# Kernel tuning notes

Measured on AMD Instinct MI355X. Metric: run time of the kernel, lower is better.

Reference implementation:

```python
import jax, jax.numpy as jnp
import numpy as np

N = 4096        # total nodes per batched graph
E_EDGES = 65536 # edges per graph (avg degree 16)
B = 16          # graphs in batch
NFEAT = 1280
NHID = 512
NHEAD = 8
DFF = 2048      # TransformerEncoderLayer default dim_feedforward
HD = NHID // NHEAD
LN_EPS = 1e-5


def setup_inputs() -> dict:
    key = jax.random.key(0)
    ks = jax.random.split(key, 32)
    s = 0.02
    inp = {}
    inp["fea1"] = jax.random.normal(ks[0], (N, NFEAT), jnp.float32)
    inp["fea2"] = jax.random.normal(ks[1], (N, NFEAT), jnp.float32)
    inp["src1"] = jax.random.randint(ks[2], (E_EDGES,), 0, N, jnp.int32)
    inp["dst1"] = jax.random.randint(ks[3], (E_EDGES,), 0, N, jnp.int32)
    inp["src2"] = jax.random.randint(ks[4], (E_EDGES,), 0, N, jnp.int32)
    inp["dst2"] = jax.random.randint(ks[5], (E_EDGES,), 0, N, jnp.int32)
    seg = ((jnp.arange(N) * B) // N).astype(jnp.int32)  # equal-size graphs, sorted ids
    inp["seg1"] = seg
    inp["seg2"] = seg
    inp["num_graphs"] = B
    # GraphConv params (torch Linear convention: y = x @ W.T + b)
    inp["W1"] = jax.random.normal(ks[6], (NHID, NFEAT), jnp.float32) * s
    inp["b1"] = jnp.zeros((NHID,), jnp.float32)
    inp["W2"] = jax.random.normal(ks[7], (NHID, NHID), jnp.float32) * s
    inp["b2"] = jnp.zeros((NHID,), jnp.float32)
    # TransformerEncoderLayer params
    inp["in_proj_w"] = jax.random.normal(ks[8], (3 * NHID, NHID), jnp.float32) * s
    inp["in_proj_b"] = jnp.zeros((3 * NHID,), jnp.float32)
    inp["out_proj_w"] = jax.random.normal(ks[9], (NHID, NHID), jnp.float32) * s
    inp["out_proj_b"] = jnp.zeros((NHID,), jnp.float32)
    inp["ln1_g"] = jnp.ones((NHID,), jnp.float32)
    inp["ln1_b"] = jnp.zeros((NHID,), jnp.float32)
    inp["ln2_g"] = jnp.ones((NHID,), jnp.float32)
    inp["ln2_b"] = jnp.zeros((NHID,), jnp.float32)
    inp["ff1_w"] = jax.random.normal(ks[10], (DFF, NHID), jnp.float32) * s
    inp["ff1_b"] = jnp.zeros((DFF,), jnp.float32)
    inp["ff2_w"] = jax.random.normal(ks[11], (NHID, DFF), jnp.float32) * s
    inp["ff2_b"] = jnp.zeros((NHID,), jnp.float32)
    # MLP head
    inp["l1_w"] = jax.random.normal(ks[12], (512, NHID), jnp.float32) * s
    inp["l1_b"] = jnp.zeros((512,), jnp.float32)
    inp["l2_w"] = jax.random.normal(ks[13], (128, 512), jnp.float32) * s
    inp["l2_b"] = jnp.zeros((128,), jnp.float32)
    inp["l3_w"] = jax.random.normal(ks[14], (2, 128), jnp.float32) * s
    inp["l3_b"] = jnp.zeros((2,), jnp.float32)
    return inp


def graph_conv(fea, src, dst, W, b):
    # DGL GraphConv, norm='both': D_in^{-1/2} A D_out^{-1/2} X W + b (W applied pre-agg)
    ones = jnp.ones(src.shape[0], fea.dtype)
    deg_out = jnp.maximum(jax.ops.segment_sum(ones, src, num_segments=N), 1.0)
    deg_in = jnp.maximum(jax.ops.segment_sum(ones, dst, num_segments=N), 1.0)
    h = fea * (deg_out ** -0.5)[:, None]
    h = h @ W.T  # [N, nhid]
    agg = jax.ops.segment_sum(h[src], dst, num_segments=N)  # scatter-add over edges
    return agg * (deg_in ** -0.5)[:, None] + b


def layer_norm(x, g, b):
    mu = jnp.mean(x, -1, keepdims=True)
    var = jnp.mean((x - mu) ** 2, -1, keepdims=True)
    return (x - mu) * jax.lax.rsqrt(var + LN_EPS) * g + b


def encoder_layer(x, in_proj_w, in_proj_b, out_proj_w, out_proj_b,
                  ln1_g, ln1_b, ln2_g, ln2_b, ff1_w, ff1_b, ff2_w, ff2_b):
    # post-norm TransformerEncoderLayer, unbatched [S, E] input, eval mode (no dropout)
    qkv = x @ in_proj_w.T + in_proj_b               # [S, 3E]
    q, k, v = jnp.split(qkv, 3, axis=-1)
    S = x.shape[0]
    q = q.reshape(S, NHEAD, HD).transpose(1, 0, 2)  # [H, S, hd]
    k = k.reshape(S, NHEAD, HD).transpose(1, 0, 2)
    v = v.reshape(S, NHEAD, HD).transpose(1, 0, 2)
    scores = jnp.einsum('hqd,hkd->hqk', q, k) / jnp.sqrt(jnp.float32(HD))
    attn = jax.nn.softmax(scores, axis=-1)
    ctx = jnp.einsum('hqk,hkd->hqd', attn, v).transpose(1, 0, 2).reshape(S, NHID)
    x = layer_norm(x + (ctx @ out_proj_w.T + out_proj_b), ln1_g, ln1_b)
    ff = jax.nn.relu(x @ ff1_w.T + ff1_b) @ ff2_w.T + ff2_b
    return layer_norm(x + ff, ln2_g, ln2_b)


def mean_nodes(fea, seg, num_graphs):
    counts = jnp.maximum(jax.ops.segment_sum(jnp.ones(fea.shape[0], fea.dtype), seg, num_segments=num_graphs), 1.0)
    return jax.ops.segment_sum(fea, seg, num_segments=num_graphs) / counts[:, None]


def reference(fea1, fea2, W1, b1, W2, b2, in_proj_w, in_proj_b, out_proj_w, out_proj_b,
              ln1_g, ln1_b, ln2_g, ln2_b, ff1_w, ff1_b, ff2_w, ff2_b,
              l1_w, l1_b, l2_w, l2_b, l3_w, l3_b,
              src1, dst1, src2, dst2, seg1, seg2, num_graphs):
    tparams = (in_proj_w, in_proj_b, out_proj_w, out_proj_b,
               ln1_g, ln1_b, ln2_g, ln2_b, ff1_w, ff1_b, ff2_w, ff2_b)
    h1 = jax.nn.relu(graph_conv(fea1, src1, dst1, W1, b1))
    h2 = jax.nn.relu(graph_conv(fea2, src2, dst2, W1, b1))
    h1 = encoder_layer(h1, *tparams)
    h2 = encoder_layer(h2, *tparams)
    h1 = jax.nn.relu(graph_conv(h1, src1, dst1, W2, b2))
    h2 = jax.nn.relu(graph_conv(h2, src2, dst2, W2, b2))
    hg = mean_nodes(h1, seg1, num_graphs) * mean_nodes(h2, seg2, num_graphs)  # [B, nhid]
    out = hg @ l1_w.T + l1_b          # note: original has NO activation between l1/l2/l3
    out = out @ l2_w.T + l2_b
    return jax.nn.softmax(out @ l3_w.T + l3_b, axis=-1)
```

## Files before the change

kernel.cpp:

```cpp
#include <hip/hip_runtime.h>
#include <math.h>

#define NN 4096
#define EE 65536
#define NS 8192
#define NFEAT 1280
#define NHID 512
#define DFF 2048

typedef unsigned short u16;
typedef unsigned int u32;
typedef __attribute__((ext_vector_type(8))) short bf16x8;
typedef __attribute__((ext_vector_type(4))) float f32x4;
#define MFMA16(A,B,C) __builtin_amdgcn_mfma_f32_16x16x32_bf16(A,B,C,0,0,0)
#define GAS __attribute__((address_space(1)))
#define LAS __attribute__((address_space(3)))

static const size_t OFF_A   = 0ull;
static const size_t OFF_HP  = 8388608ull;
static const size_t OFF_X   = 12582912ull;
static const size_t OFF_XB  = 16777216ull;
static const size_t OFF_E   = 18874368ull;
static const size_t OFF_VT  = 25165824ull;
static const size_t OFF_CTB = 27262976ull;
static const size_t OFF_W1B = 29360128ull;
static const size_t OFF_IPB = 29687808ull;
static const size_t OFF_OPB = 30081024ull;
static const size_t OFF_F1B = 30212096ull;
static const size_t OFF_F2B = 30736384ull;
static const size_t OFF_W2B = 31260672ull;
static const size_t OFF_ME  = 31391744ull;
static const size_t OFF_DG  = 31408128ull;
static const size_t OFF_INT = 31424512ull;

#define IH_S1 0
#define IH_D1 4096
#define IH_S2 8192
#define IH_D2 12288
#define IO_F1 16384
#define IO_F2 20608
#define IC_1  24832
#define IC_2  28928
#define IE_1  33024
#define IE_2  98560

__device__ __forceinline__ u16 f2b(float x) {
    u32 u = __float_as_uint(x);
    return (u16)((u + 0x7fffu + ((u >> 16) & 1u)) >> 16);
}
__device__ __forceinline__ float b_lo(u32 u) { return __uint_as_float(u << 16); }
__device__ __forceinline__ float b_hi(u32 u) { return __uint_as_float(u & 0xffff0000u); }

__global__ __launch_bounds__(256) void k_hist(const int* __restrict__ s1, const int* __restrict__ d1,
                                              const int* __restrict__ s2, const int* __restrict__ d2,
                                              int* __restrict__ I)
{
    int e = blockIdx.x * 256 + threadIdx.x;
    if (e < EE) {
        atomicAdd(&I[IH_S1 + s1[e]], 1);
        atomicAdd(&I[IH_D1 + d1[e]], 1);
        atomicAdd(&I[IH_S2 + s2[e]], 1);
        atomicAdd(&I[IH_D2 + d2[e]], 1);
    }
}

__global__ __launch_bounds__(256) void k_deg_fin(const int* __restrict__ I, float* __restrict__ deg)
{
    int i = blockIdx.x * 256 + threadIdx.x;
    if (i < 4 * NN) deg[i] = rsqrtf(fmaxf((float)I[i], 1.0f));
}

__global__ __launch_bounds__(256) void k_scan(int* __restrict__ I)
{
    int b = blockIdx.x;
    const int* hist = I + (b ? IH_D2 : IH_D1);
    int* offs = I + (b ? IO_F2 : IO_F1);
    int* cur  = I + (b ? IC_2 : IC_1);
    __shared__ int part[256];
    int t = threadIdx.x;
    int base = t * 16;
    int loc[16];
    int s = 0;
#pragma unroll
    for (int i = 0; i < 16; ++i) { loc[i] = s; s += hist[base + i]; }
    part[t] = s;
    __syncthreads();
    if (t == 0) {
        int a = 0;
        for (int i = 0; i < 256; ++i) { int v = part[i]; part[i] = a; a += v; }
        offs[NN] = a;
    }
    __syncthreads();
    int p = part[t];
#pragma unroll
    for (int i = 0; i < 16; ++i) { offs[base + i] = p + loc[i]; cur[base + i] = p + loc[i]; }
}

__global__ __launch_bounds__(256) void k_fill(const int* __restrict__ s1, const int* __restrict__ d1,
                                              const int* __restrict__ s2, const int* __restrict__ d2,
                                              int* __restrict__ I)
{
    int e = blockIdx.x * 256 + threadIdx.x;
    if (e < EE) {
        int p1 = atomicAdd(&I[IC_1 + d1[e]], 1);
        I[IE_1 + p1] = s1[e];
        int p2 = atomicAdd(&I[IC_2 + d2[e]], 1);
        I[IE_2 + p2] = s2[e];
    }
}

__global__ __launch_bounds__(256) void k_cvt(const float* __restrict__ src, u16* __restrict__ dst, int n)
{
    int i = (blockIdx.x * 256 + threadIdx.x) * 8;
    if (i >= n) return;
    float4 a = *(const float4*)&src[i];
    float4 b = *(const float4*)&src[i + 4];
    uint4 o;
    o.x = (u32)f2b(a.x) | ((u32)f2b(a.y) << 16);
    o.y = (u32)f2b(a.z) | ((u32)f2b(a.w) << 16);
    o.z = (u32)f2b(b.x) | ((u32)f2b(b.y) << 16);
    o.w = (u32)f2b(b.z) | ((u32)f2b(b.w) << 16);
    *(uint4*)&dst[i] = o;
}

__global__ __launch_bounds__(256) void k_scale_bf(const float* __restrict__ in1, const float* __restrict__ in2,
                                                  const float* __restrict__ sc1, const float* __restrict__ sc2,
                                                  u16* __restrict__ out, int ncol)
{
    int quads = ncol >> 2;
    long long idx = (long long)blockIdx.x * 256 + threadIdx.x;
    if (idx >= (long long)NS * quads) return;
    int r  = (int)(idx / quads);
    int cq = (int)(idx % quads) * 4;
    const float* in; const float* sc; int rr;
    if (r < NN) { in = in1; sc = sc1; rr = r; } else { in = in2; sc = sc2; rr = r - NN; }
    float4 v = *(const float4*)&in[(size_t)rr * ncol + cq];
    float s = sc[rr];
    uint2 o;
    o.x = (u32)f2b(v.x * s) | ((u32)f2b(v.y * s) << 16);
    o.y = (u32)f2b(v.z * s) | ((u32)f2b(v.w * s) << 16);
    *(uint2*)&out[(size_t)r * ncol + cq] = o;
}

__global__ __launch_bounds__(256) void k_gemm_bf(const u16* __restrict__ A, const u16* __restrict__ W,
                                                 const float* __restrict__ bias, float* __restrict__ Cf,
                                                 u16* __restrict__ Cb, int M, int N, int K, int relu)
{
    __shared__ u16 As[128 * 32];
    __shared__ u16 Bs[128 * 32];
    int t = threadIdx.x;
    int w = t >> 6, L = t & 63;
    int lm = L & 15, lq = L >> 4;
    int wr = w >> 1, wc = w & 1;
    int row0 = blockIdx.y * 128, col0 = blockIdx.x * 128;
    f32x4 acc[4][4];
#pragma unroll
    for (int i = 0; i < 4; ++i)
#pragma unroll
        for (int j = 0; j < 4; ++j) acc[i][j] = (f32x4){0.f, 0.f, 0.f, 0.f};

    int sr = t >> 2;
    int sk = (t & 3) * 8;
    const u16* Ag = &A[(size_t)row0 * K + sk];
    const u16* Wg = &W[(size_t)col0 * K + sk];

    for (int k0 = 0; k0 < K; k0 += 32) {
        uint4 a0 = *(const uint4*)&Ag[(size_t)sr * K + k0];
        uint4 a1 = *(const uint4*)&Ag[(size_t)(sr + 64) * K + k0];
        uint4 b0 = *(const uint4*)&Wg[(size_t)sr * K + k0];
        uint4 b1 = *(const uint4*)&Wg[(size_t)(sr + 64) * K + k0];
        __syncthreads();
        *(uint4*)&As[sr * 32 + sk] = a0;
        *(uint4*)&As[(sr + 64) * 32 + sk] = a1;
        *(uint4*)&Bs[sr * 32 + sk] = b0;
        *(uint4*)&Bs[(sr + 64) * 32 + sk] = b1;
        __syncthreads();
        bf16x8 af[4], bw[4];
#pragma unroll
        for (int i = 0; i < 4; ++i) {
            af[i] = *(const bf16x8*)&As[(wr * 64 + i * 16 + lm) * 32 + lq * 8];
            bw[i] = *(const bf16x8*)&Bs[(wc * 64 + i * 16 + lm) * 32 + lq * 8];
        }
#pragma unroll
        for (int i = 0; i < 4; ++i)
#pragma unroll
            for (int j = 0; j < 4; ++j)
                acc[i][j] = MFMA16(af[i], bw[j], acc[i][j]);
    }

#pragma unroll
    for (int i = 0; i < 4; ++i) {
        int row = row0 + wr * 64 + i * 16 + lq * 4;
#pragma unroll
        for (int j = 0; j < 4; ++j) {
            int col = col0 + wc * 64 + j * 16 + lm;
            float bv = bias ? bias[col] : 0.0f;
#pragma unroll
            for (int r = 0; r < 4; ++r) {
                float v = acc[i][j][r] + bv;
                if (relu) v = fmaxf(v, 0.0f);
                size_t off = (size_t)(row + r) * N + col;
                if (Cb) Cb[off] = f2b(v);
                else    Cf[off] = v;
            }
        }
    }
}

__global__ __launch_bounds__(256) void k_gather_bf(const u16* __restrict__ hp, const int* __restrict__ I,
                                                   const float* __restrict__ din1, const float* __restrict__ din2,
                                                   const float* __restrict__ bias,
                                                   float* __restrict__ xout, u16* __restrict__ xb)
{
    int r = blockIdx.x, c = threadIdx.x;
    int g = r >> 12, rl = r & (NN - 1);
    const int* off = I + (g ? IO_F2 : IO_F1);
    const int* eid = I + (g ? IE_2 : IE_1);
    int beg = off[rl], end = off[rl + 1];
    const u16* base = hp + ((size_t)g << 12) * NHID;
    float a0 = 0.f, a1 = 0.f;
    for (int i = beg; i < end; ++i) {
        u32 v = ((const u32*)(base + (size_t)eid[i] * NHID))[c];
        a0 += b_lo(v);
        a1 += b_hi(v);
    }
    float s = (g ? din2 : din1)[rl];
    float2 bv = *(const float2*)&bias[c * 2];
    float v0 = fmaxf(fmaf(a0, s, bv.x), 0.f);
    float v1 = fmaxf(fmaf(a1, s, bv.y), 0.f);
    size_t o = (size_t)r * NHID + c * 2;
    if (xout) *(float2*)&xout[o] = make_float2(v0, v1);
    if (xb) *(u32*)&xb[o] = (u32)f2b(v0) | ((u32)f2b(v1) << 16);
}

__global__ __launch_bounds__(256) void k_vtrans(const u16* __restrict__ qkvb, u16* __restrict__ vtb)
{
    __shared__ u16 tile[64][65];
    int t = threadIdx.x;
    int kt = blockIdx.x, h = blockIdx.y, g = blockIdx.z;
    int k0 = kt * 64;
    size_t gbase = (size_t)g * NN;
#pragma unroll
    for (int p = 0; p < 4; ++p) {
        int kl = p * 16 + (t >> 4);
        int d  = (t & 15) * 4;
        uint2 v = *(const uint2*)&qkvb[(gbase + k0 + kl) * 1536 + 1024 + h * 64 + d];
        tile[kl][d + 0] = (u16)(v.x & 0xffff);
        tile[kl][d + 1] = (u16)(v.x >> 16);
        tile[kl][d + 2] = (u16)(v.y & 0xffff);
        tile[kl][d + 3] = (u16)(v.y >> 16);
    }
    __syncthreads();
#pragma unroll
    for (int p = 0; p < 4; ++p) {
        int dl = p * 16 + (t >> 4);
        int k4 = (t & 15) * 4;
        u16 v0 = tile[k4 + 0][dl];
        u16 v1 = tile[k4 + 1][dl];
        u16 v2 = tile[k4 + 2][dl];
        u16 v3 = tile[k4 + 3][dl];
        uint2 o;
        o.x = (u32)v0 | ((u32)v1 << 16);
        o.y = (u32)v2 | ((u32)v3 << 16);
        *(uint2*)&vtb[((size_t)(g * 8 + h) * 64 + dl) * (size_t)NN + k0 + k4] = o;
    }
}

__global__ __launch_bounds__(256, 2) void k_attn(const u16* __restrict__ qkv,
                                                 const u16* __restrict__ vt,
                                                 u16* __restrict__ ctb)
{
    __shared__ __align__(16) u16 Kl[2][32 * 64];
    __shared__ __align__(16) u16 Vl[2][64 * 32];
    __shared__ __align__(16) u16 Pl[4][32 * 40];
    int t = threadIdx.x;
    int w = t >> 6, L = t & 63;
    int lm = L & 15, lq = L >> 4;
    int qt = blockIdx.x, h = blockIdx.y, g = blockIdx.z;
    size_t gbase = (size_t)g * NN;
    int q0 = qt * 128 + w * 32;

    const u16* kbase = &qkv[gbase * 1536 + 512 + h * 64];
    const u16* vbase = &vt[(size_t)(g * 8 + h) * 64 * (size_t)NN];

    int krow = t >> 3;
    int kbyt = ((t & 7) * 16) ^ ((krow & 7) << 4);
    const u16* kg = &kbase[(size_t)krow * 1536 + (kbyt >> 1)];
    int vrow = t >> 2;
    int vbyt = ((t & 3) * 16) ^ ((vrow & 3) << 4);
    const u16* vg = &vbase[(size_t)vrow * NN + (vbyt >> 1)];
    u16* Pw = &Pl[w][0];

    bf16x8 qa[2][2];
#pragma unroll
    for (int qg = 0; qg < 2; ++qg) {
        const u16* qp = &qkv[(gbase + q0 + qg * 16 + lm) * 1536 + h * 64 + lq * 8];
        qa[qg][0] = *(const bf16x8*)qp;
        qa[qg][1] = *(const bf16x8*)(qp + 32);
    }
    f32x4 ctx[2][4];
#pragma unroll
    for (int qg = 0; qg < 2; ++qg)
#pragma unroll
        for (int n = 0; n < 4; ++n) ctx[qg][n] = (f32x4){0.f, 0.f, 0.f, 0.f};
    float m[2][4], lsum[2][4];
#pragma unroll
    for (int qg = 0; qg < 2; ++qg)
#pragma unroll
        for (int r = 0; r < 4; ++r) { m[qg][r] = -1e30f; lsum[qg][r] = 0.0f; }

    __builtin_amdgcn_global_load_lds((const GAS void*)kg, (LAS void*)((LAS char*)&Kl[0][0] + w * 1024), 16, 0, 0);
    __builtin_amdgcn_global_load_lds((const GAS void*)vg, (LAS void*)((LAS char*)&Vl[0][0] + w * 1024), 16, 0, 0);
    __syncthreads();

    int cur = 0;
    for (int t0 = 0; t0 < NN; t0 += 32) {
        if (t0 + 32 < NN) {
            __builtin_amdgcn_global_load_lds((const GAS void*)(kg + (size_t)(t0 + 32) * 1536),
                                             (LAS void*)((LAS char*)&Kl[cur ^ 1][0] + w * 1024), 16, 0, 0);
            __builtin_amdgcn_global_load_lds((const GAS void*)(vg + (t0 + 32)),
                                             (LAS void*)((LAS char*)&Vl[cur ^ 1][0] + w * 1024), 16, 0, 0);
        }
        const char* Kc = (const char*)&Kl[cur][0];
        const char* Vc = (const char*)&Vl[cur][0];
        bf16x8 kb[2][2], vb[4];
#pragma unroll
        for (int kc = 0; kc < 2; ++kc) {
            int row = kc * 16 + lm;
            int sw = (row & 7) << 4;
            const char* rp = Kc + row * 128;
            kb[kc][0] = *(const bf16x8*)(rp + ((lq * 16) ^ sw));
            kb[kc][1] = *(const bf16x8*)(rp + ((64 + lq * 16) ^ sw));
        }
#pragma unroll
        for (int n = 0; n < 4; ++n) {
            int row = n * 16 + lm;
            vb[n] = *(const bf16x8*)(Vc + row * 64 + ((lq * 16) ^ ((row & 3) << 4)));
        }

        f32x4 s[2][2];
        __builtin_amdgcn_s_setprio(1);
#pragma unroll
        for (int kc = 0; kc < 2; ++kc)
#pragma unroll
            for (int qg = 0; qg < 2; ++qg) {
                f32x4 z = (f32x4){0.f, 0.f, 0.f, 0.f};
                z = MFMA16(qa[qg][0], kb[kc][0], z);
                z = MFMA16(qa[qg][1], kb[kc][1], z);
                s[qg][kc] = z * 0.125f;
            }
        __builtin_amdgcn_s_setprio(0);

        float dmax = -1e30f;
#pragma unroll
        for (int qg = 0; qg < 2; ++qg)
#pragma unroll
            for (int r = 0; r < 4; ++r)
                dmax = fmaxf(dmax, fmaxf(s[qg][0][r], s[qg][1][r]) - m[qg][r]);
        if (__any(dmax > 8.0f)) {
#pragma unroll
            for (int qg = 0; qg < 2; ++qg)
#pragma unroll
                for (int r = 0; r < 4; ++r) {
                    float mr = fmaxf(s[qg][0][r], s[qg][1][r]);
                    mr = fmaxf(mr, __shfl_xor(mr, 1));
                    mr = fmaxf(mr, __shfl_xor(mr, 2));
                    mr = fmaxf(mr, __shfl_xor(mr, 4));
                    mr = fmaxf(mr, __shfl_xor(mr, 8));
                    float mn = fmaxf(m[qg][r], mr);
                    float corr = __expf(m[qg][r] - mn);
                    m[qg][r] = mn;
                    lsum[qg][r] *= corr;
#pragma unroll
                    for (int n = 0; n < 4; ++n) ctx[qg][n][r] *= corr;
                }
        }
#pragma unroll
        for (int qg = 0; qg < 2; ++qg)
#pragma unroll
            for (int r = 0; r < 4; ++r) {
                float p0 = __expf(s[qg][0][r] - m[qg][r]);
                float p1 = __expf(s[qg][1][r] - m[qg][r]);
                lsum[qg][r] += p0 + p1;
                int row = qg * 16 + lq * 4 + r;
                Pw[row * 40 + lm] = f2b(p0);
                Pw[row * 40 + 16 + lm] = f2b(p1);
            }

        __builtin_amdgcn_s_setprio(1);
#pragma unroll
        for (int qg = 0; qg < 2; ++qg) {
            bf16x8 pa = *(const bf16x8*)&Pw[(qg * 16 + lm) * 40 + lq * 8];
#pragma unroll
            for (int n = 0; n < 4; ++n)
                ctx[qg][n] = MFMA16(pa, vb[n], ctx[qg][n]);
        }
        __builtin_amdgcn_s_setprio(0);

        __syncthreads();
        cur ^= 1;
    }

#pragma unroll
    for (int qg = 0; qg < 2; ++qg) {
        float inv[4];
#pragma unroll
        for (int r = 0; r < 4; ++r) {
            float lr = lsum[qg][r];
            lr += __shfl_xor(lr, 1);
            lr += __shfl_xor(lr, 2);
            lr += __shfl_xor(lr, 4);
            lr += __shfl_xor(lr, 8);
            inv[r] = 1.0f / lr;
        }
#pragma unroll
        for (int n = 0; n < 4; ++n)
#pragma unroll
            for (int r = 0; r < 4; ++r) {
                int row = q0 + qg * 16 + lq * 4 + r;
                int col = h * 64 + n * 16 + lm;
                ctb[(gbase + row) * NHID + col] = f2b(ctx[qg][n][r] * inv[r]);
            }
    }
}

__global__ __launch_bounds__(256) void k_add_ln(const float* __restrict__ x, const float* __restrict__ y,
                                                const float* __restrict__ g, const float* __restrict__ bb,
                                                float* __restrict__ xout, u16* __restrict__ xb,
                                                const float* __restrict__ sc1, const float* __restrict__ sc2)
{
    int r = blockIdx.x, tid = threadIdx.x;
    int c = tid * 2;
    float2 xv = *(const float2*)&x[(size_t)r * NHID + c];
    float2 yv = *(const float2*)&y[(size_t)r * NHID + c];
    float a0 = xv.x + yv.x, a1 = xv.y + yv.y;
    float s = a0 + a1;
    float qs = a0 * a0 + a1 * a1;
#pragma unroll
    for (int off = 32; off > 0; off >>= 1) {
        s  += __shfl_xor(s, off);
        qs += __shfl_xor(qs, off);
    }
    __shared__ float ss[4], qq[4];
    int w = tid >> 6;
    if ((tid & 63) == 0) { ss[w] = s; qq[w] = qs; }
    __syncthreads();
    s  = ss[0] + ss[1] + ss[2] + ss[3];
    qs = qq[0] + qq[1] + qq[2] + qq[3];
    float mu  = s * (1.0f / NHID);
    float var = qs * (1.0f / NHID) - mu * mu;
    float rs = rsqrtf(var + 1e-5f);
    float2 gv = *(const float2*)&g[c];
    float2 bv = *(const float2*)&bb[c];
    float o0 = (a0 - mu) * rs * gv.x + bv.x;
    float o1 = (a1 - mu) * rs * gv.y + bv.y;
    if (xout) *(float2*)&xout[(size_t)r * NHID + c] = make_float2(o0, o1);
    float sc = 1.0f;
    if (sc1) sc = (r < NN) ? sc1[r] : sc2[r - NN];
    u32 o = (u32)f2b(o0 * sc) | ((u32)f2b(o1 * sc) << 16);
    *(u32*)&xb[(size_t)r * NHID + c] = o;
}

__global__ __launch_bounds__(512) void k_seg_mean(const float* __restrict__ h, float* __restrict__ means)
{
    int b = blockIdx.x;
    int st = blockIdx.y;
    int col = threadIdx.x;
    const float* hp = &h[((size_t)st * NN + (size_t)b * 256) * NHID + col];
    float acc = 0.0f;
    for (int i = 0; i < 256; ++i) acc += hp[(size_t)i * NHID];
    means[((size_t)st * 16 + b) * NHID + col] = acc * (1.0f / 256.0f);
}

__global__ __launch_bounds__(256) void k_head(const float* __restrict__ means,
                                              const float* __restrict__ l1w, const float* __restrict__ l1b,
                                              const float* __restrict__ l2w, const float* __restrict__ l2b,
                                              const float* __restrict__ l3w, const float* __restrict__ l3b,
                                              float* __restrict__ out)
{
    __shared__ float hg[512];
    __shared__ float t1[512];
    __shared__ float t2[128];
    int b = blockIdx.x;
    int t = threadIdx.x;
    hg[t]       = means[b * 512 + t]       * means[(16 + b) * 512 + t];
    hg[t + 256] = means[b * 512 + t + 256] * means[(16 + b) * 512 + t + 256];
    __syncthreads();
#pragma unroll
    for (int o = t; o < 512; o += 256) {
        const float* wr = &l1w[(size_t)o * 512];
        float acc = l1b[o];
        for (int k = 0; k < 512; k += 4) {
            float4 w = *(const float4*)&wr[k];
            acc = fmaf(hg[k], w.x, acc);
            acc = fmaf(hg[k + 1], w.y, acc);
            acc = fmaf(hg[k + 2], w.z, acc);
            acc = fmaf(hg[k + 3], w.w, acc);
        }
        t1[o] = acc;
    }
    __syncthreads();
    if (t < 128) {
        const float* wr = &l2w[(size_t)t * 512];
        float acc = l2b[t];
        for (int k = 0; k < 512; k += 4) {
            float4 w = *(const float4*)&wr[k];
            acc = fmaf(t1[k], w.x, acc);
            acc = fmaf(t1[k + 1], w.y, acc);
            acc = fmaf(t1[k + 2], w.z, acc);
            acc = fmaf(t1[k + 3], w.w, acc);
        }
        t2[t] = acc;
    }
    __syncthreads();
    if (t < 64) {
        float p0 = t2[t] * l3w[t] + t2[t + 64] * l3w[t + 64];
        float p1 = t2[t] * l3w[128 + t] + t2[t + 64] * l3w[128 + t + 64];
#pragma unroll
        for (int off = 32; off > 0; off >>= 1) {
            p0 += __shfl_xor(p0, off);
            p1 += __shfl_xor(p1, off);
        }
        if (t == 0) {
            float v0 = p0 + l3b[0], v1 = p1 + l3b[1];
            float mx = fmaxf(v0, v1);
            float e0 = __expf(v0 - mx), e1 = __expf(v1 - mx);
            float inv = 1.0f / (e0 + e1);
            out[b * 2 + 0] = e0 * inv;
            out[b * 2 + 1] = e1 * inv;
        }
    }
}

extern "C" void kernel_launch(void* const* d_in, const int* in_sizes, int n_in,
                              void* d_out, int out_size, void* d_ws, size_t ws_size,
                              hipStream_t stream)
{
    const float* fea1 = (const float*)d_in[0];
    const float* fea2 = (const float*)d_in[1];
    const int* src1 = (const int*)d_in[2];
    const int* dst1 = (const int*)d_in[3];
    const int* src2 = (const int*)d_in[4];
    const int* dst2 = (const int*)d_in[5];
    const float* W1 = (const float*)d_in[9];
    const float* b1 = (const float*)d_in[10];
    const float* W2 = (const float*)d_in[11];
    const float* b2 = (const float*)d_in[12];
    const float* in_proj_w = (const float*)d_in[13];
    const float* in_proj_b = (const float*)d_in[14];
    const float* out_proj_w = (const float*)d_in[15];
    const float* out_proj_b = (const float*)d_in[16];
    const float* ln1_g = (const float*)d_in[17];
    const float* ln1_b = (const float*)d_in[18];
    const float* ln2_g = (const float*)d_in[19];
    const float* ln2_b = (const float*)d_in[20];
    const float* ff1_w = (const float*)d_in[21];
    const float* ff1_b = (const float*)d_in[22];
    const float* ff2_w = (const float*)d_in[23];
    const float* ff2_b = (const float*)d_in[24];
    const float* l1_w = (const float*)d_in[25];
    const float* l1_b = (const float*)d_in[26];
    const float* l2_w = (const float*)d_in[27];
    const float* l2_b = (const float*)d_in[28];
    const float* l3_w = (const float*)d_in[29];
    const float* l3_b = (const float*)d_in[30];

    float* ws = (float*)d_ws;
    u16*  Ab   = (u16*)(ws + OFF_A);
    float* HP  = ws + OFF_HP;
    u16*  HPb  = (u16*)(ws + OFF_HP);
    float* X   = ws + OFF_X;
    u16*  Xb   = (u16*)(ws + OFF_XB);
    u16*  QKVb = (u16*)(ws + OFF_E);
    float* AG2 = ws + OFF_E;
    u16*  Vtb  = (u16*)(ws + OFF_VT);
    u16*  CTb  = (u16*)(ws + OFF_CTB);
    u16*  W1b  = (u16*)(ws + OFF_W1B);
    u16*  IPb  = (u16*)(ws + OFF_IPB);
    u16*  OPb  = (u16*)(ws + OFF_OPB);
    u16*  F1b  = (u16*)(ws + OFF_F1B);
    u16*  F2b  = (u16*)(ws + OFF_F2B);
    u16*  W2b  = (u16*)(ws + OFF_W2B);
    float* ME  = ws + OFF_ME;
    float* DG  = ws + OFF_DG;
    int*   I   = (int*)(ws + OFF_INT);
    float* dout1 = DG;
    float* din1  = DG + NN;
    float* dout2 = DG + 2 * NN;
    float* din2  = DG + 3 * NN;

    hipMemsetAsync(I, 0, 4 * NN * sizeof(int), stream);

    k_hist<<<EE / 256, 256, 0, stream>>>(src1, dst1, src2, dst2, I);
    k_deg_fin<<<(4 * NN) / 256, 256, 0, stream>>>(I, DG);
    k_scan<<<2, 256, 0, stream>>>(I);
    k_fill<<<EE / 256, 256, 0, stream>>>(src1, dst1, src2, dst2, I);

    k_cvt<<<(NHID * NFEAT / 8 + 255) / 256, 256, 0, stream>>>(W1, W1b, NHID * NFEAT);
    k_cvt<<<(3 * NHID * NHID / 8 + 255) / 256, 256, 0, stream>>>(in_proj_w, IPb, 3 * NHID * NHID);
    k_cvt<<<(NHID * NHID / 8 + 255) / 256, 256, 0, stream>>>(out_proj_w, OPb, NHID * NHID);
    k_cvt<<<(DFF * NHID / 8 + 255) / 256, 256, 0, stream>>>(ff1_w, F1b, DFF * NHID);
    k_cvt<<<(NHID * DFF / 8 + 255) / 256, 256, 0, stream>>>(ff2_w, F2b, NHID * DFF);
    k_cvt<<<(NHID * NHID / 8 + 255) / 256, 256, 0, stream>>>(W2, W2b, NHID * NHID);

    {
        long long tq = (long long)NS * (NFEAT / 4);
        k_scale_bf<<<(int)((tq + 255) / 256), 256, 0, stream>>>(fea1, fea2, dout1, dout2, Ab, NFEAT);
    }
    k_gemm_bf<<<dim3(NHID / 128, NS / 128), 256, 0, stream>>>(Ab, W1b, nullptr, nullptr, HPb, NS, NHID, NFEAT, 0);
    k_gather_bf<<<NS, 256, 0, stream>>>(HPb, I, din1, din2, b1, X, Xb);

    k_gemm_bf<<<dim3(1536 / 128, NS / 128), 256, 0, stream>>>(Xb, IPb, in_proj_b, nullptr, QKVb, NS, 1536, NHID, 0);
    k_vtrans<<<dim3(NN / 64, 8, 2), 256, 0, stream>>>(QKVb, Vtb);
    k_attn<<<dim3(NN / 128, 8, 2), 256, 0, stream>>>(QKVb, Vtb, CTb);
    k_gemm_bf<<<dim3(NHID / 128, NS / 128), 256, 0, stream>>>(CTb, OPb, out_proj_b, HP, nullptr, NS, NHID, NHID, 0);
    k_add_ln<<<NS, 256, 0, stream>>>(X, HP, ln1_g, ln1_b, X, Xb, nullptr, nullptr);
    k_gemm_bf<<<dim3(DFF / 128, NS / 128), 256, 0, stream>>>(Xb, F1b, ff1_b, nullptr, Ab, NS, DFF, NHID, 1);
    k_gemm_bf<<<dim3(NHID / 128, NS / 128), 256, 0, stream>>>(Ab, F2b, ff2_b, HP, nullptr, NS, NHID, DFF, 0);
    k_add_ln<<<NS, 256, 0, stream>>>(X, HP, ln2_g, ln2_b, nullptr, Ab, dout1, dout2);

    k_gemm_bf<<<dim3(NHID / 128, NS / 128), 256, 0, stream>>>(Ab, W2b, nullptr, nullptr, HPb, NS, NHID, NHID, 0);
    k_gather_bf<<<NS, 256, 0, stream>>>(HPb, I, din1, din2, b2, AG2, nullptr);

    k_seg_mean<<<dim3(16, 2), 512, 0, stream>>>(AG2, ME);
    k_head<<<16, 256, 0, stream>>>(ME, l1_w, l1_b, l2_w, l2_b, l3_w, l3_b, (float*)d_out);
}
```

Measured before the change: 674.7 us.

## Widen attention KV tile, use exp2 softmax, async LDS GEMM loads, 64-wide tiles

The attention kernel now processes 64 keys per iteration instead of 32. It folds log2(e) into the score scale so it can use exp2f, and writes P with packed bf16 stores into a swizzled 128-byte-row layout. The GEMM switches from register-staged LDS stores to global_load_lds direct copies and gains a BN=64 template variant, used for the N=512 outputs to put more blocks on the GPU. The V transpose reorders keys to match the new K/V staging layout. The aim is fewer barriers and loop overheads plus better occupancy, at the cost of more LDS per attention block and a GEMM that is still single-buffered.

```diff
diff --git a/kernel.cpp b/kernel.cpp
--- a/kernel.cpp
+++ b/kernel.cpp
@@ -1,4 +1,5 @@
 #include <hip/hip_runtime.h>
+#include <hip/hip_bf16.h>
 #include <math.h>
 
 #define NN 4096
@@ -15,6 +16,9 @@
 #define MFMA16(A,B,C) __builtin_amdgcn_mfma_f32_16x16x32_bf16(A,B,C,0,0,0)
 #define GAS __attribute__((address_space(1)))
 #define LAS __attribute__((address_space(3)))
+
+#define SCL 0.18033688011112042f
+#define THR 11.541560327111707f
 
 static const size_t OFF_A   = 0ull;
 static const size_t OFF_HP  = 8388608ull;
@@ -142,55 +146,58 @@
     *(uint2*)&out[(size_t)r * ncol + cq] = o;
 }
 
+template<int BN>
 __global__ __launch_bounds__(256) void k_gemm_bf(const u16* __restrict__ A, const u16* __restrict__ W,
                                                  const float* __restrict__ bias, float* __restrict__ Cf,
                                                  u16* __restrict__ Cb, int M, int N, int K, int relu)
 {
+    constexpr int RM = (BN == 128) ? 4 : 2;
     __shared__ u16 As[128 * 32];
-    __shared__ u16 Bs[128 * 32];
+    __shared__ u16 Bs[BN * 32];
     int t = threadIdx.x;
     int w = t >> 6, L = t & 63;
     int lm = L & 15, lq = L >> 4;
-    int wr = w >> 1, wc = w & 1;
-    int row0 = blockIdx.y * 128, col0 = blockIdx.x * 128;
-    f32x4 acc[4][4];
-#pragma unroll
-    for (int i = 0; i < 4; ++i)
+    int wr = (BN == 128) ? (w >> 1) : w;
+    int wc = (BN == 128) ? (w & 1) : 0;
+    int row0 = blockIdx.y * 128, col0 = blockIdx.x * BN;
+    f32x4 acc[RM][4];
+#pragma unroll
+    for (int i = 0; i < RM; ++i)
 #pragma unroll
         for (int j = 0; j < 4; ++j) acc[i][j] = (f32x4){0.f, 0.f, 0.f, 0.f};
 
-    int sr = t >> 2;
-    int sk = (t & 3) * 8;
-    const u16* Ag = &A[(size_t)row0 * K + sk];
-    const u16* Wg = &W[(size_t)col0 * K + sk];
+    const u16* As0 = &A[(size_t)(row0 + (w * 2) * 16 + (L >> 2)) * K + (L & 3) * 8];
+    const u16* As1 = As0 + (size_t)16 * K;
+    const u16* Bs0 = &W[(size_t)(col0 + ((BN == 128) ? (w * 2) * 16 : w * 16) + (L >> 2)) * K + (L & 3) * 8];
+    const u16* Bs1 = Bs0 + (size_t)16 * K;
+    u16* AsW = &As[(w * 2) * 512];
+    u16* BsW = (BN == 128) ? &Bs[(w * 2) * 512] : &Bs[w * 512];
 
     for (int k0 = 0; k0 < K; k0 += 32) {
-        uint4 a0 = *(const uint4*)&Ag[(size_t)sr * K + k0];
-        uint4 a1 = *(const uint4*)&Ag[(size_t)(sr + 64) * K + k0];
-        uint4 b0 = *(const uint4*)&Wg[(size_t)sr * K + k0];
-        uint4 b1 = *(const uint4*)&Wg[(size_t)(sr + 64) * K + k0];
+        if (k0) __syncthreads();
+        __builtin_amdgcn_global_load_lds((const GAS void*)(As0 + k0), (LAS void*)(LAS char*)AsW, 16, 0, 0);
+        __builtin_amdgcn_global_load_lds((const GAS void*)(As1 + k0), (LAS void*)((LAS char*)AsW + 1024), 16, 0, 0);
+        __builtin_amdgcn_global_load_lds((const GAS void*)(Bs0 + k0), (LAS void*)(LAS char*)BsW, 16, 0, 0);
+        if constexpr (BN == 128)
+            __builtin_amdgcn_global_load_lds((const GAS void*)(Bs1 + k0), (LAS void*)((LAS char*)BsW + 1024), 16, 0, 0);
         __syncthreads();
-        *(uint4*)&As[sr * 32 + sk] = a0;
-        *(uint4*)&As[(sr + 64) * 32 + sk] = a1;
-        *(uint4*)&Bs[sr * 32 + sk] = b0;
-        *(uint4*)&Bs[(sr + 64) * 32 + sk] = b1;
-        __syncthreads();
-        bf16x8 af[4], bw[4];
-#pragma unroll
-        for (int i = 0; i < 4; ++i) {
-            af[i] = *(const bf16x8*)&As[(wr * 64 + i * 16 + lm) * 32 + lq * 8];
-            bw[i] = *(const bf16x8*)&Bs[(wc * 64 + i * 16 + lm) * 32 + lq * 8];
-        }
-#pragma unroll
-        for (int i = 0; i < 4; ++i)
+        bf16x8 af[RM], bw[4];
+#pragma unroll
+        for (int i = 0; i < RM; ++i)
+            af[i] = *(const bf16x8*)&As[(wr * (RM * 16) + i * 16 + lm) * 32 + lq * 8];
+#pragma unroll
+        for (int j = 0; j < 4; ++j)
+            bw[j] = *(const bf16x8*)&Bs[(wc * 64 + j * 16 + lm) * 32 + lq * 8];
+#pragma unroll
+        for (int i = 0; i < RM; ++i)
 #pragma unroll
             for (int j = 0; j < 4; ++j)
                 acc[i][j] = MFMA16(af[i], bw[j], acc[i][j]);
     }
 
 #pragma unroll
-    for (int i = 0; i < 4; ++i) {
-        int row = row0 + wr * 64 + i * 16 + lq * 4;
+    for (int i = 0; i < RM; ++i) {
+        int row = row0 + wr * (RM * 16) + i * 16 + lq * 4;
 #pragma unroll
         for (int j = 0; j < 4; ++j) {
             int col = col0 + wc * 64 + j * 16 + lm;
@@ -254,15 +261,15 @@
 #pragma unroll
     for (int p = 0; p < 4; ++p) {
         int dl = p * 16 + (t >> 4);
-        int k4 = (t & 15) * 4;
-        u16 v0 = tile[k4 + 0][dl];
-        u16 v1 = tile[k4 + 1][dl];
-        u16 v2 = tile[k4 + 2][dl];
-        u16 v3 = tile[k4 + 3][dl];
+        int kap = (t & 15) * 4;
+        u16 v0 = tile[(t & 15) + 0][dl];
+        u16 v1 = tile[(t & 15) + 16][dl];
+        u16 v2 = tile[(t & 15) + 32][dl];
+        u16 v3 = tile[(t & 15) + 48][dl];
         uint2 o;
         o.x = (u32)v0 | ((u32)v1 << 16);
         o.y = (u32)v2 | ((u32)v3 << 16);
-        *(uint2*)&vtb[((size_t)(g * 8 + h) * 64 + dl) * (size_t)NN + k0 + k4] = o;
+        *(uint2*)&vtb[((size_t)(g * 8 + h) * 64 + dl) * (size_t)NN + k0 + kap] = o;
     }
 }
 
@@ -270,9 +277,9 @@
                                                  const u16* __restrict__ vt,
                                                  u16* __restrict__ ctb)
 {
-    __shared__ __align__(16) u16 Kl[2][32 * 64];
-    __shared__ __align__(16) u16 Vl[2][64 * 32];
-    __shared__ __align__(16) u16 Pl[4][32 * 40];
+    __shared__ __align__(16) u16 Kl[2][64 * 64];
+    __shared__ __align__(16) u16 Vl[2][64 * 64];
+    __shared__ __align__(16) u16 Pl[4][32 * 64];
     int t = threadIdx.x;
     int w = t >> 6, L = t & 63;
     int lm = L & 15, lq = L >> 4;
@@ -283,12 +290,15 @@
     const u16* kbase = &qkv[gbase * 1536 + 512 + h * 64];
     const u16* vbase = &vt[(size_t)(g * 8 + h) * 64 * (size_t)NN];
 
-    int krow = t >> 3;
-    int kbyt = ((t & 7) * 16) ^ ((krow & 7) << 4);
-    const u16* kg = &kbase[(size_t)krow * 1536 + (kbyt >> 1)];
-    int vrow = t >> 2;
-    int vbyt = ((t & 3) * 16) ^ ((vrow & 3) << 4);
-    const u16* vg = &vbase[(size_t)vrow * NN + (vbyt >> 1)];
+    int srcb = ((L & 7) * 16) ^ ((L >> 3) << 4);
+    int rho0 = (w * 2) * 8 + (L >> 3);
+    int rho1 = rho0 + 8;
+    int kp0 = (rho0 & 15) * 4 + (rho0 >> 4);
+    int kp1 = (rho1 & 15) * 4 + (rho1 >> 4);
+    const u16* kg0 = &kbase[(size_t)kp0 * 1536 + (srcb >> 1)];
+    const u16* kg1 = &kbase[(size_t)kp1 * 1536 + (srcb >> 1)];
+    const u16* vg0 = &vbase[(size_t)rho0 * NN + (srcb >> 1)];
+    const u16* vg1 = &vbase[(size_t)rho1 * NN + (srcb >> 1)];
     u16* Pw = &Pl[w][0];
 
     bf16x8 qa[2][2];
@@ -309,66 +319,62 @@
 #pragma unroll
         for (int r = 0; r < 4; ++r) { m[qg][r] = -1e30f; lsum[qg][r] = 0.0f; }
 
-    __builtin_amdgcn_global_load_lds((const GAS void*)kg, (LAS void*)((LAS char*)&Kl[0][0] + w * 1024), 16, 0, 0);
-    __builtin_amdgcn_global_load_lds((const GAS void*)vg, (LAS void*)((LAS char*)&Vl[0][0] + w * 1024), 16, 0, 0);
+    __builtin_amdgcn_global_load_lds((const GAS void*)kg0, (LAS void*)((LAS char*)&Kl[0][0] + (w * 2) * 1024), 16, 0, 0);
+    __builtin_amdgcn_global_load_lds((const GAS void*)kg1, (LAS void*)((LAS char*)&Kl[0][0] + (w * 2 + 1) * 1024), 16, 0, 0);
+    __builtin_amdgcn_global_load_lds((const GAS void*)vg0, (LAS void*)((LAS char*)&Vl[0][0] + (w * 2) * 1024), 16, 0, 0);
+    __builtin_amdgcn_global_load_lds((const GAS void*)vg1, (LAS void*)((LAS char*)&Vl[0][0] + (w * 2 + 1) * 1024), 16, 0, 0);
     __syncthreads();
 
     int cur = 0;
-    for (int t0 = 0; t0 < NN; t0 += 32) {
-        if (t0 + 32 < NN) {
-            __builtin_amdgcn_global_load_lds((const GAS void*)(kg + (size_t)(t0 + 32) * 1536),
-                                             (LAS void*)((LAS char*)&Kl[cur ^ 1][0] + w * 1024), 16, 0, 0);
-            __builtin_amdgcn_global_load_lds((const GAS void*)(vg + (t0 + 32)),
-                                             (LAS void*)((LAS char*)&Vl[cur ^ 1][0] + w * 1024), 16, 0, 0);
+    for (int t0 = 0; t0 < NN; t0 += 64) {
+        if (t0 + 64 < NN) {
+            size_t ko = (size_t)(t0 + 64) * 1536;
+            __builtin_amdgcn_global_load_lds((const GAS void*)(kg0 + ko), (LAS void*)((LAS char*)&Kl[cur ^ 1][0] + (w * 2) * 1024), 16, 0, 0);
+            __builtin_amdgcn_global_load_lds((const GAS void*)(kg1 + ko), (LAS void*)((LAS char*)&Kl[cur ^ 1][0] + (w * 2 + 1) * 1024), 16, 0, 0);
+            __builtin_amdgcn_global_load_lds((const GAS void*)(vg0 + t0 + 64), (LAS void*)((LAS char*)&Vl[cur ^ 1][0] + (w * 2) * 1024), 16, 0, 0);
+            __builtin_amdgcn_global_load_lds((const GAS void*)(vg1 + t0 + 64), (LAS void*)((LAS char*)&Vl[cur ^ 1][0] + (w * 2 + 1) * 1024), 16, 0, 0);
         }
         const char* Kc = (const char*)&Kl[cur][0];
         const char* Vc = (const char*)&Vl[cur][0];
-        bf16x8 kb[2][2], vb[4];
-#pragma unroll
-        for (int kc = 0; kc < 2; ++kc) {
-            int row = kc * 16 + lm;
-            int sw = (row & 7) << 4;
-            const char* rp = Kc + row * 128;
-            kb[kc][0] = *(const bf16x8*)(rp + ((lq * 16) ^ sw));
-            kb[kc][1] = *(const bf16x8*)(rp + ((64 + lq * 16) ^ sw));
-        }
-#pragma unroll
-        for (int n = 0; n < 4; ++n) {
-            int row = n * 16 + lm;
-            vb[n] = *(const bf16x8*)(Vc + row * 64 + ((lq * 16) ^ ((row & 3) << 4)));
-        }
-
-        f32x4 s[2][2];
+        int sw = (lm & 7) << 4;
+
+        f32x4 s[2][4];
         __builtin_amdgcn_s_setprio(1);
 #pragma unroll
-        for (int kc = 0; kc < 2; ++kc)
+        for (int kc = 0; kc < 4; ++kc) {
+            const char* rp = Kc + (kc * 16 + lm) * 128;
+            bf16x8 kb0 = *(const bf16x8*)(rp + ((lq * 16) ^ sw));
+            bf16x8 kb1 = *(const bf16x8*)(rp + ((64 + lq * 16) ^ sw));
 #pragma unroll
             for (int qg = 0; qg < 2; ++qg) {
                 f32x4 z = (f32x4){0.f, 0.f, 0.f, 0.f};
-                z = MFMA16(qa[qg][0], kb[kc][0], z);
-                z = MFMA16(qa[qg][1], kb[kc][1], z);
-                s[qg][kc] = z * 0.125f;
+                z = MFMA16(qa[qg][0], kb0, z);
+                z = MFMA16(qa[qg][1], kb1, z);
+                s[qg][kc] = z * SCL;
             }
+        }
         __builtin_amdgcn_s_setprio(0);
 
         float dmax = -1e30f;
 #pragma unroll
         for (int qg = 0; qg < 2; ++qg)
 #pragma unroll
-            for (int r = 0; r < 4; ++r)
-                dmax = fmaxf(dmax, fmaxf(s[qg][0][r], s[qg][1][r]) - m[qg][r]);
-        if (__any(dmax > 8.0f)) {
+            for (int r = 0; r < 4; ++r) {
+                float a = fmaxf(fmaxf(s[qg][0][r], s[qg][1][r]), fmaxf(s[qg][2][r], s[qg][3][r]));
+                dmax = fmaxf(dmax, a - m[qg][r]);
+            }
+        if (__any(dmax > THR)) {
 #pragma unroll
             for (int qg = 0; qg < 2; ++qg)
 #pragma unroll
                 for (int r = 0; r < 4; ++r) {
-                    float mr = fmaxf(s[qg][0][r], s[qg][1][r]);
+                    float mr = fmaxf(fmaxf(s[qg][0][r], s[qg][1][r]), fmaxf(s[qg][2][r], s[qg][3][r]));
                     mr = fmaxf(mr, __shfl_xor(mr, 1));
                     mr = fmaxf(mr, __shfl_xor(mr, 2));
                     mr = fmaxf(mr, __shfl_xor(mr, 4));
                     mr = fmaxf(mr, __shfl_xor(mr, 8));
                     float mn = fmaxf(m[qg][r], mr);
-                    float corr = __expf(m[qg][r] - mn);
+                    float corr = exp2f(m[qg][r] - mn);
                     m[qg][r] = mn;
                     lsum[qg][r] *= corr;
 #pragma unroll
@@ -379,21 +385,39 @@
         for (int qg = 0; qg < 2; ++qg)
 #pragma unroll
             for (int r = 0; r < 4; ++r) {
-                float p0 = __expf(s[qg][0][r] - m[qg][r]);
-                float p1 = __expf(s[qg][1][r] - m[qg][r]);
-                lsum[qg][r] += p0 + p1;
+                float mq = m[qg][r];
+                float p0 = exp2f(s[qg][0][r] - mq);
+                float p1 = exp2f(s[qg][1][r] - mq);
+                float p2 = exp2f(s[qg][2][r] - mq);
+                float p3 = exp2f(s[qg][3][r] - mq);
+                lsum[qg][r] += (p0 + p1) + (p2 + p3);
                 int row = qg * 16 + lq * 4 + r;
-                Pw[row * 40 + lm] = f2b(p0);
-                Pw[row * 40 + 16 + lm] = f2b(p1);
+                __hip_bfloat162 c0 = __float22bfloat162_rn(make_float2(p0, p1));
+                __hip_bfloat162 c1 = __float22bfloat162_rn(make_float2(p2, p3));
+                uint2 pv;
+                pv.x = *(u32*)&c0;
+                pv.y = *(u32*)&c1;
+                *(uint2*)((char*)Pw + row * 128 + ((lm * 8) ^ ((row & 7) << 4))) = pv;
             }
 
         __builtin_amdgcn_s_setprio(1);
+        bf16x8 vbf[4][2];
+#pragma unroll
+        for (int n = 0; n < 4; ++n) {
+            const char* vr = Vc + (n * 16 + lm) * 128;
+            vbf[n][0] = *(const bf16x8*)(vr + ((lq * 16) ^ sw));
+            vbf[n][1] = *(const bf16x8*)(vr + ((64 + lq * 16) ^ sw));
+        }
 #pragma unroll
         for (int qg = 0; qg < 2; ++qg) {
-            bf16x8 pa = *(const bf16x8*)&Pw[(qg * 16 + lm) * 40 + lq * 8];
-#pragma unroll
-            for (int n = 0; n < 4; ++n)
-                ctx[qg][n] = MFMA16(pa, vb[n], ctx[qg][n]);
+            const char* pr = (const char*)Pw + (qg * 16 + lm) * 128;
+            bf16x8 pa0 = *(const bf16x8*)(pr + ((lq * 16) ^ sw));
+            bf16x8 pa1 = *(const bf16x8*)(pr + ((64 + lq * 16) ^ sw));
+#pragma unroll
+            for (int n = 0; n < 4; ++n) {
+                ctx[qg][n] = MFMA16(pa0, vbf[n][0], ctx[qg][n]);
+                ctx[qg][n] = MFMA16(pa1, vbf[n][1], ctx[qg][n]);
+            }
         }
         __builtin_amdgcn_s_setprio(0);
 
@@ -607,19 +631,19 @@
         long long tq = (long long)NS * (NFEAT / 4);
         k_scale_bf<<<(int)((tq + 255) / 256), 256, 0, stream>>>(fea1, fea2, dout1, dout2, Ab, NFEAT);
     }
-    k_gemm_bf<<<dim3(NHID / 128, NS / 128), 256, 0, stream>>>(Ab, W1b, nullptr, nullptr, HPb, NS, NHID, NFEAT, 0);
+    k_gemm_bf<64><<<dim3(NHID / 64, NS / 128), 256, 0, stream>>>(Ab, W1b, nullptr, nullptr, HPb, NS, NHID, NFEAT, 0);
     k_gather_bf<<<NS, 256, 0, stream>>>(HPb, I, din1, din2, b1, X, Xb);
 
-    k_gemm_bf<<<dim3(1536 / 128, NS / 128), 256, 0, stream>>>(Xb, IPb, in_proj_b, nullptr, QKVb, NS, 1536, NHID, 0);
+    k_gemm_bf<128><<<dim3(1536 / 128, NS / 128), 256, 0, stream>>>(Xb, IPb, in_proj_b, nullptr, QKVb, NS, 1536, NHID, 0);
     k_vtrans<<<dim3(NN / 64, 8, 2), 256, 0, stream>>>(QKVb, Vtb);
     k_attn<<<dim3(NN / 128, 8, 2), 256, 0, stream>>>(QKVb, Vtb, CTb);
-    k_gemm_bf<<<dim3(NHID / 128, NS / 128), 256, 0, stream>>>(CTb, OPb, out_proj_b, HP, nullptr, NS, NHID, NHID, 0);
+    k_gemm_bf<64><<<dim3(NHID / 64, NS / 128), 256, 0, stream>>>(CTb, OPb, out_proj_b, HP, nullptr, NS, NHID, NHID, 0);
     k_add_ln<<<NS, 256, 0, stream>>>(X, HP, ln1_g, ln1_b, X, Xb, nullptr, nullptr);
-    k_gemm_bf<<<dim3(DFF / 128, NS / 128), 256, 0, stream>>>(Xb, F1b, ff1_b, nullptr, Ab, NS, DFF, NHID, 1);
-    k_gemm_bf<<<dim3(NHID / 128, NS / 128), 256, 0, stream>>>(Ab, F2b, ff2_b, HP, nullptr, NS, NHID, DFF, 0);
+    k_gemm_bf<128><<<dim3(DFF / 128, NS / 128), 256, 0, stream>>>(Xb, F1b, ff1_b, nullptr, Ab, NS, DFF, NHID, 1);
+    k_gemm_bf<64><<<dim3(NHID / 64, NS / 128), 256, 0, stream>>>(Ab, F2b, ff2_b, HP, nullptr, NS, NHID, DFF, 0);
     k_add_ln<<<NS, 256, 0, stream>>>(X, HP, ln2_g, ln2_b, nullptr, Ab, dout1, dout2);
 
-    k_gemm_bf<<<dim3(NHID / 128, NS / 128), 256, 0, stream>>>(Ab, W2b, nullptr, nullptr, HPb, NS, NHID, NHID, 0);
+    k_gemm_bf<64><<<dim3(NHID / 64, NS / 128), 256, 0, stream>>>(Ab, W2b, nullptr, nullptr, HPb, NS, NHID, NHID, 0);
     k_gather_bf<<<NS, 256, 0, stream>>>(HPb, I, din1, din2, b2, AG2, nullptr);
 
     k_seg_mean<<<dim3(16, 2), 512, 0, stream>>>(AG2, ME);
```

After: 628.8 us. 1.07x faster.
